# Optimization experiments

Measured on AMD Instinct MI355X. Metric: run time of the kernel, lower is better.

The kernel has to match this reference:

```python
import jax, jax.numpy as jnp
import numpy as np

B, S, D = 4, 4096, 1024
DFF = 4 * D
ACTIVE = 1024  # ceil(S * 0.25)


def setup_inputs() -> dict:
    key = jax.random.key(0)
    ks = jax.random.split(key, 4)
    x = jax.random.normal(ks[0], (B, S, D), dtype=jnp.float32)
    rw = jax.random.normal(ks[1], (D,), dtype=jnp.float32) * 0.02
    rb = jnp.zeros((1,), dtype=jnp.float32)
    w1 = jax.random.normal(ks[2], (D, DFF), dtype=jnp.float32) * 0.02
    b1 = jnp.zeros((DFF,), dtype=jnp.float32)
    w2 = jax.random.normal(ks[3], (DFF, D), dtype=jnp.float32) * 0.02
    b2 = jnp.zeros((D,), dtype=jnp.float32)
    return {"x": x, "rw": rw, "rb": rb, "w1": w1, "b1": b1,
            "w2": w2, "b2": b2, "active_tokens": ACTIVE}


def reference(x, rw, rb, w1, b1, w2, b2, active_tokens):
    b, s, d = x.shape
    # router: Linear(n_embd, 1) -> [B, S] scores
    scores = jnp.einsum('bsd,d->bs', x, rw) + rb[0]
    # top-k tokens per batch row
    _, idx = jax.lax.top_k(scores, active_tokens)          # [B, K] int32
    sel = jnp.take_along_axis(x, idx[..., None], axis=1)   # [B, K, D]
    # dense MLP on selected tokens (exact GELU as in torch nn.GELU)
    h = jax.nn.gelu(jnp.einsum('bkd,df->bkf', sel, w1) + b1, approximate=False)
    out = jnp.einsum('bkf,fd->bkd', h, w2) + b2            # [B, K, D]
    # sigmoid gate from router scores of selected tokens
    gates = jax.nn.sigmoid(jnp.take_along_axis(scores, idx, axis=1))  # [B, K]
    out = out * gates[..., None]
    # scatter back into zeros at selected positions
    flat_idx = (idx + jnp.arange(b, dtype=idx.dtype)[:, None] * s).reshape(-1)
    flat_out = jnp.zeros((b * s, d), dtype=out.dtype)
    flat_out = flat_out.at[flat_idx].set(out.reshape(-1, d))
    return flat_out.reshape(b, s, d)
```

## Files before the change

kernel.cpp:

```cpp
#include <hip/hip_runtime.h>
#include <hip/hip_bf16.h>
#include <cstdint>
#include <cstddef>

#define Bz 4
#define Sz 4096
#define Dz 1024
#define DFFz 4096
#define KACT 1024

typedef __bf16 bf16;
typedef __attribute__((ext_vector_type(8))) __bf16 bf16x8;
typedef __attribute__((ext_vector_type(4))) float f32x4;

__device__ __forceinline__ void async16(const void* g, void* l) {
  __builtin_amdgcn_global_load_lds(
      (const __attribute__((address_space(1))) void*)g,
      (__attribute__((address_space(3))) void*)l, 16, 0, 0);
}

__global__ void zero_out_k(float4* __restrict__ out, int n4) {
  int i = blockIdx.x * blockDim.x + threadIdx.x;
  int stride = gridDim.x * blockDim.x;
  for (; i < n4; i += stride) out[i] = make_float4(0.f, 0.f, 0.f, 0.f);
}

__global__ void router_k(const float* __restrict__ x, const float* __restrict__ rw,
                         const float* __restrict__ rb, float* __restrict__ scores) {
  int row = blockIdx.x * 4 + (threadIdx.x >> 6);
  int lane = threadIdx.x & 63;
  const float4* xr = (const float4*)(x + (size_t)row * Dz);
  const float4* wr = (const float4*)rw;
  float acc = 0.f;
#pragma unroll
  for (int i = 0; i < 4; ++i) {
    float4 a = xr[lane + i * 64];
    float4 w = wr[lane + i * 64];
    acc += a.x * w.x + a.y * w.y + a.z * w.z + a.w * w.w;
  }
#pragma unroll
  for (int d = 32; d; d >>= 1) acc += __shfl_down(acc, d, 64);
  if (lane == 0) scores[row] = acc + rb[0];
}

__global__ void transpose_cvt(const float* __restrict__ in, bf16* __restrict__ out,
                              int R, int C) {
  __shared__ float t[32][33];
  int c0 = blockIdx.x * 32, r0 = blockIdx.y * 32;
  int tx = threadIdx.x, ty = threadIdx.y;
#pragma unroll
  for (int i = 0; i < 32; i += 8) t[ty + i][tx] = in[(size_t)(r0 + ty + i) * C + c0 + tx];
  __syncthreads();
#pragma unroll
  for (int i = 0; i < 32; i += 8)
    out[(size_t)(c0 + ty + i) * R + r0 + tx] = (bf16)t[tx][ty + i];
}

__global__ void select_gather_k(const float* __restrict__ x, const float* __restrict__ scores,
                                int* __restrict__ cnt, int* __restrict__ sel_idx,
                                float* __restrict__ gates, bf16* __restrict__ Xsel) {
  int b = blockIdx.x >> 12;
  int s = blockIdx.x & (Sz - 1);
  const float* sc = scores + (size_t)b * Sz;
  float mine = sc[s];
  int tid = threadIdx.x;
  int c = 0;
  for (int t = tid; t < Sz; t += 256) {
    float o = sc[t];
    c += (o > mine) || (o == mine && t < s);
  }
#pragma unroll
  for (int d = 32; d; d >>= 1) c += __shfl_down(c, d, 64);
  __shared__ int red[4];
  __shared__ int rowbase;
  if ((tid & 63) == 0) red[tid >> 6] = c;
  __syncthreads();
  if (tid == 0) {
    int tot = red[0] + red[1] + red[2] + red[3];
    if (tot < KACT) {
      int pos = atomicAdd(cnt + b, 1);
      int m = b * KACT + pos;
      sel_idx[m] = s;
      gates[m] = 1.f / (1.f + expf(-mine));
      rowbase = m;
    } else {
      rowbase = -1;
    }
  }
  __syncthreads();
  int m = rowbase;
  if (m >= 0) {
    const float* xr = x + ((size_t)b * Sz + s) * Dz;
    bf16* xd = Xsel + (size_t)m * Dz;
    for (int i = tid; i < Dz; i += 256) xd[i] = (bf16)xr[i];
  }
}

__global__ __launch_bounds__(256) void gemm1_k(const bf16* __restrict__ A,
                                               const bf16* __restrict__ Bt,
                                               const float* __restrict__ bias,
                                               bf16* __restrict__ H) {
  constexpr int K = Dz, N = DFFz;
  __shared__ __align__(16) bf16 As[128 * 32];
  __shared__ __align__(16) bf16 Bs[128 * 32];
  const int tid = threadIdx.x;
  const int wave = tid >> 6, lane = tid & 63;
  const int quad = lane >> 4, l16 = lane & 15;
  const int m0 = blockIdx.y * 128, n0 = blockIdx.x * 128;
  const int wm = (wave >> 1) * 64, wn = (wave & 1) * 64;
  const int r0 = tid >> 2;
  const int kk = (tid & 3) * 8;

  f32x4 acc[4][4] = {};

  const bf16* Ag = A + (size_t)(m0 + r0) * K + kk;
  const bf16* Bg = Bt + (size_t)(n0 + r0) * K + kk;
  bf16* lAs0 = &As[wave * 512];
  bf16* lAs1 = &As[2048 + wave * 512];
  bf16* lBs0 = &Bs[wave * 512];
  bf16* lBs1 = &Bs[2048 + wave * 512];

  for (int k0 = 0; k0 < K; k0 += 32) {
    async16(Ag + k0, lAs0);
    async16(Ag + (size_t)64 * K + k0, lAs1);
    async16(Bg + k0, lBs0);
    async16(Bg + (size_t)64 * K + k0, lBs1);
    __syncthreads();
    bf16x8 af[4], bfr[4];
#pragma unroll
    for (int i = 0; i < 4; ++i) {
      af[i] = *(const bf16x8*)&As[(wm + i * 16 + l16) * 32 + quad * 8];
      bfr[i] = *(const bf16x8*)&Bs[(wn + i * 16 + l16) * 32 + quad * 8];
    }
#pragma unroll
    for (int mi = 0; mi < 4; ++mi)
#pragma unroll
      for (int ni = 0; ni < 4; ++ni)
        acc[mi][ni] = __builtin_amdgcn_mfma_f32_16x16x32_bf16(af[mi], bfr[ni], acc[mi][ni], 0, 0, 0);
    __syncthreads();
  }

#pragma unroll
  for (int mi = 0; mi < 4; ++mi) {
    int mbase = m0 + wm + mi * 16 + quad * 4;
#pragma unroll
    for (int ni = 0; ni < 4; ++ni) {
      int n = n0 + wn + ni * 16 + l16;
      float bn = bias[n];
#pragma unroll
      for (int r = 0; r < 4; ++r) {
        float z = acc[mi][ni][r] + bn;
        float g = 0.5f * z * (1.f + erff(z * 0.70710678118654752f));
        H[(size_t)(mbase + r) * N + n] = (bf16)g;
      }
    }
  }
}

__global__ __launch_bounds__(256) void gemm2_k(const bf16* __restrict__ A,
                                               const bf16* __restrict__ Bt,
                                               const float* __restrict__ bias,
                                               const int* __restrict__ sel_idx,
                                               const float* __restrict__ gates,
                                               float* __restrict__ out) {
  constexpr int K = DFFz, N = Dz;
  __shared__ __align__(16) bf16 As[128 * 32];
  __shared__ __align__(16) bf16 Bs[128 * 32];
  const int tid = threadIdx.x;
  const int wave = tid >> 6, lane = tid & 63;
  const int quad = lane >> 4, l16 = lane & 15;
  const int m0 = blockIdx.y * 128, n0 = blockIdx.x * 128;
  const int wm = (wave >> 1) * 64, wn = (wave & 1) * 64;
  const int r0 = tid >> 2;
  const int kk = (tid & 3) * 8;

  f32x4 acc[4][4] = {};

  const bf16* Ag = A + (size_t)(m0 + r0) * K + kk;
  const bf16* Bg = Bt + (size_t)(n0 + r0) * K + kk;
  bf16* lAs0 = &As[wave * 512];
  bf16* lAs1 = &As[2048 + wave * 512];
  bf16* lBs0 = &Bs[wave * 512];
  bf16* lBs1 = &Bs[2048 + wave * 512];

  for (int k0 = 0; k0 < K; k0 += 32) {
    async16(Ag + k0, lAs0);
    async16(Ag + (size_t)64 * K + k0, lAs1);
    async16(Bg + k0, lBs0);
    async16(Bg + (size_t)64 * K + k0, lBs1);
    __syncthreads();
    bf16x8 af[4], bfr[4];
#pragma unroll
    for (int i = 0; i < 4; ++i) {
      af[i] = *(const bf16x8*)&As[(wm + i * 16 + l16) * 32 + quad * 8];
      bfr[i] = *(const bf16x8*)&Bs[(wn + i * 16 + l16) * 32 + quad * 8];
    }
#pragma unroll
    for (int mi = 0; mi < 4; ++mi)
#pragma unroll
      for (int ni = 0; ni < 4; ++ni)
        acc[mi][ni] = __builtin_amdgcn_mfma_f32_16x16x32_bf16(af[mi], bfr[ni], acc[mi][ni], 0, 0, 0);
    __syncthreads();
  }

#pragma unroll
  for (int mi = 0; mi < 4; ++mi) {
#pragma unroll
    for (int r = 0; r < 4; ++r) {
      int m = m0 + wm + mi * 16 + quad * 4 + r;
      int b = m >> 10;
      int s = sel_idx[m];
      float gt = gates[m];
      float* orow = out + ((size_t)b * Sz + s) * Dz;
#pragma unroll
      for (int ni = 0; ni < 4; ++ni) {
        int n = n0 + wn + ni * 16 + l16;
        orow[n] = (acc[mi][ni][r] + bias[n]) * gt;
      }
    }
  }
}

extern "C" void kernel_launch(void* const* d_in, const int* in_sizes, int n_in,
                              void* d_out, int out_size, void* d_ws, size_t ws_size,
                              hipStream_t stream) {
  (void)in_sizes; (void)n_in; (void)out_size; (void)ws_size;
  const float* x  = (const float*)d_in[0];
  const float* rw = (const float*)d_in[1];
  const float* rb = (const float*)d_in[2];
  const float* w1 = (const float*)d_in[3];
  const float* b1 = (const float*)d_in[4];
  const float* w2 = (const float*)d_in[5];
  const float* b2 = (const float*)d_in[6];
  float* out = (float*)d_out;

  char* ws = (char*)d_ws;
  float* scores = (float*)ws;  ws += (size_t)Bz * Sz * 4;
  int*   sel_idx = (int*)ws;   ws += (size_t)Bz * KACT * 4;
  float* gates = (float*)ws;   ws += (size_t)Bz * KACT * 4;
  int*   cnt = (int*)ws;       ws += 256;
  bf16*  w1T = (bf16*)ws;      ws += (size_t)DFFz * Dz * 2;
  bf16*  w2T = (bf16*)ws;      ws += (size_t)Dz * DFFz * 2;
  bf16*  Xsel = (bf16*)ws;     ws += (size_t)Bz * KACT * Dz * 2;
  bf16*  H = (bf16*)ws;        ws += (size_t)Bz * KACT * DFFz * 2;

  hipMemsetAsync(cnt, 0, 16, stream);
  zero_out_k<<<8192, 256, 0, stream>>>((float4*)out, (Bz * Sz * Dz) / 4);
  router_k<<<(Bz * Sz) / 4, 256, 0, stream>>>(x, rw, rb, scores);
  transpose_cvt<<<dim3(DFFz / 32, Dz / 32), dim3(32, 8), 0, stream>>>(w1, w1T, Dz, DFFz);
  transpose_cvt<<<dim3(Dz / 32, DFFz / 32), dim3(32, 8), 0, stream>>>(w2, w2T, DFFz, Dz);
  select_gather_k<<<Bz * Sz, 256, 0, stream>>>(x, scores, cnt, sel_idx, gates, Xsel);
  gemm1_k<<<dim3(DFFz / 128, (Bz * KACT) / 128), 256, 0, stream>>>(Xsel, w1T, b1, H);
  gemm2_k<<<dim3(Dz / 128, (Bz * KACT) / 128), 256, 0, stream>>>(H, w2T, b2, sel_idx, gates, out);
}
```

Before: 358.6 us.

## Double-buffer GEMM LDS tiles and use rank-based slots in select_gather

The two GEMM kernels now use double-buffered LDS tiles. The next k-tile's async global-to-LDS loads are issued before computing on the current tile, with explicit vmcnt waits and barriers, so load latency overlaps the MFMA work. select_gather_k drops the atomic counter and its memset: each selected token writes to slot b*K + rank, and the row copy is vectorised to float4 loads and bf16x4 stores. LDS use per GEMM block doubles, and the hand-written waitcnt/barrier sequence depends on the compiler emitting the loads in the expected order.

New measurement: 352.4 us. Within noise of the previous version (-1.7%).

```diff
diff --git a/kernel.cpp b/kernel.cpp
--- a/kernel.cpp
+++ b/kernel.cpp
@@ -11,6 +11,7 @@
 
 typedef __bf16 bf16;
 typedef __attribute__((ext_vector_type(8))) __bf16 bf16x8;
+typedef __attribute__((ext_vector_type(4))) __bf16 bf16x4;
 typedef __attribute__((ext_vector_type(4))) float f32x4;
 
 __device__ __forceinline__ void async16(const void* g, void* l) {
@@ -57,8 +58,8 @@
 }
 
 __global__ void select_gather_k(const float* __restrict__ x, const float* __restrict__ scores,
-                                int* __restrict__ cnt, int* __restrict__ sel_idx,
-                                float* __restrict__ gates, bf16* __restrict__ Xsel) {
+                                int* __restrict__ sel_idx, float* __restrict__ gates,
+                                bf16* __restrict__ Xsel) {
   int b = blockIdx.x >> 12;
   int s = blockIdx.x & (Sz - 1);
   const float* sc = scores + (size_t)b * Sz;
@@ -72,74 +73,75 @@
 #pragma unroll
   for (int d = 32; d; d >>= 1) c += __shfl_down(c, d, 64);
   __shared__ int red[4];
-  __shared__ int rowbase;
   if ((tid & 63) == 0) red[tid >> 6] = c;
   __syncthreads();
+  int tot = red[0] + red[1] + red[2] + red[3];
+  if (tot >= KACT) return;
+  int m = b * KACT + tot;
   if (tid == 0) {
-    int tot = red[0] + red[1] + red[2] + red[3];
-    if (tot < KACT) {
-      int pos = atomicAdd(cnt + b, 1);
-      int m = b * KACT + pos;
-      sel_idx[m] = s;
-      gates[m] = 1.f / (1.f + expf(-mine));
-      rowbase = m;
-    } else {
-      rowbase = -1;
-    }
-  }
-  __syncthreads();
-  int m = rowbase;
-  if (m >= 0) {
-    const float* xr = x + ((size_t)b * Sz + s) * Dz;
-    bf16* xd = Xsel + (size_t)m * Dz;
-    for (int i = tid; i < Dz; i += 256) xd[i] = (bf16)xr[i];
-  }
-}
+    sel_idx[m] = s;
+    gates[m] = 1.f / (1.f + expf(-mine));
+  }
+  const float4* xr = (const float4*)(x + ((size_t)b * Sz + s) * Dz);
+  bf16x4* xd = (bf16x4*)(Xsel + (size_t)m * Dz);
+  float4 v = xr[tid];
+  bf16x4 o = {(bf16)v.x, (bf16)v.y, (bf16)v.z, (bf16)v.w};
+  xd[tid] = o;
+}
+
+#define GEMM_PREAMBLE(KV)                                                  \
+  __shared__ __align__(16) bf16 As[2][128 * 32];                           \
+  __shared__ __align__(16) bf16 Bs[2][128 * 32];                           \
+  const int tid = threadIdx.x;                                             \
+  const int wave = tid >> 6, lane = tid & 63;                              \
+  const int quad = lane >> 4, l16 = lane & 15;                             \
+  const int m0 = blockIdx.y * 128, n0 = blockIdx.x * 128;                  \
+  const int wm = (wave >> 1) * 64, wn = (wave & 1) * 64;                   \
+  const int r0 = tid >> 2;                                                 \
+  const int kk = (tid & 3) * 8;                                            \
+  f32x4 acc[4][4] = {};                                                    \
+  const bf16* Ag = A + (size_t)(m0 + r0) * KV + kk;                        \
+  const bf16* Bg = Bt + (size_t)(n0 + r0) * KV + kk;                       \
+  const int ldsoff = wave * 512;
+
+#define GEMM_ISSUE(KV, p, k0)                                              \
+  async16(Ag + (k0), &As[p][ldsoff]);                                      \
+  async16(Ag + (size_t)64 * KV + (k0), &As[p][2048 + ldsoff]);             \
+  async16(Bg + (k0), &Bs[p][ldsoff]);                                      \
+  async16(Bg + (size_t)64 * KV + (k0), &Bs[p][2048 + ldsoff]);
+
+#define GEMM_MAINLOOP(KV)                                                  \
+  GEMM_ISSUE(KV, 0, 0)                                                     \
+  int cur = 0;                                                             \
+  for (int it = 0; it < (KV) / 32; ++it) {                                 \
+    if (it + 1 < (KV) / 32) {                                              \
+      GEMM_ISSUE(KV, cur ^ 1, (it + 1) * 32)                               \
+      asm volatile("s_waitcnt vmcnt(4)\ns_barrier" ::: "memory");          \
+    } else {                                                               \
+      asm volatile("s_waitcnt vmcnt(0)\ns_barrier" ::: "memory");          \
+    }                                                                      \
+    bf16x8 af[4], bfr[4];                                                  \
+    _Pragma("unroll")                                                      \
+    for (int i = 0; i < 4; ++i) {                                          \
+      af[i] = *(const bf16x8*)&As[cur][(wm + i * 16 + l16) * 32 + quad * 8]; \
+      bfr[i] = *(const bf16x8*)&Bs[cur][(wn + i * 16 + l16) * 32 + quad * 8]; \
+    }                                                                      \
+    _Pragma("unroll")                                                      \
+    for (int mi = 0; mi < 4; ++mi)                                         \
+      _Pragma("unroll")                                                    \
+      for (int ni = 0; ni < 4; ++ni)                                       \
+        acc[mi][ni] = __builtin_amdgcn_mfma_f32_16x16x32_bf16(af[mi], bfr[ni], acc[mi][ni], 0, 0, 0); \
+    asm volatile("s_waitcnt lgkmcnt(0)\ns_barrier" ::: "memory");          \
+    cur ^= 1;                                                              \
+  }
 
 __global__ __launch_bounds__(256) void gemm1_k(const bf16* __restrict__ A,
                                                const bf16* __restrict__ Bt,
                                                const float* __restrict__ bias,
                                                bf16* __restrict__ H) {
   constexpr int K = Dz, N = DFFz;
-  __shared__ __align__(16) bf16 As[128 * 32];
-  __shared__ __align__(16) bf16 Bs[128 * 32];
-  const int tid = threadIdx.x;
-  const int wave = tid >> 6, lane = tid & 63;
-  const int quad = lane >> 4, l16 = lane & 15;
-  const int m0 = blockIdx.y * 128, n0 = blockIdx.x * 128;
-  const int wm = (wave >> 1) * 64, wn = (wave & 1) * 64;
-  const int r0 = tid >> 2;
-  const int kk = (tid & 3) * 8;
-
-  f32x4 acc[4][4] = {};
-
-  const bf16* Ag = A + (size_t)(m0 + r0) * K + kk;
-  const bf16* Bg = Bt + (size_t)(n0 + r0) * K + kk;
-  bf16* lAs0 = &As[wave * 512];
-  bf16* lAs1 = &As[2048 + wave * 512];
-  bf16* lBs0 = &Bs[wave * 512];
-  bf16* lBs1 = &Bs[2048 + wave * 512];
-
-  for (int k0 = 0; k0 < K; k0 += 32) {
-    async16(Ag + k0, lAs0);
-    async16(Ag + (size_t)64 * K + k0, lAs1);
-    async16(Bg + k0, lBs0);
-    async16(Bg + (size_t)64 * K + k0, lBs1);
-    __syncthreads();
-    bf16x8 af[4], bfr[4];
-#pragma unroll
-    for (int i = 0; i < 4; ++i) {
-      af[i] = *(const bf16x8*)&As[(wm + i * 16 + l16) * 32 + quad * 8];
-      bfr[i] = *(const bf16x8*)&Bs[(wn + i * 16 + l16) * 32 + quad * 8];
-    }
-#pragma unroll
-    for (int mi = 0; mi < 4; ++mi)
-#pragma unroll
-      for (int ni = 0; ni < 4; ++ni)
-        acc[mi][ni] = __builtin_amdgcn_mfma_f32_16x16x32_bf16(af[mi], bfr[ni], acc[mi][ni], 0, 0, 0);
-    __syncthreads();
-  }
-
+  GEMM_PREAMBLE(K)
+  GEMM_MAINLOOP(K)
 #pragma unroll
   for (int mi = 0; mi < 4; ++mi) {
     int mbase = m0 + wm + mi * 16 + quad * 4;
@@ -163,46 +165,9 @@
                                                const int* __restrict__ sel_idx,
                                                const float* __restrict__ gates,
                                                float* __restrict__ out) {
-  constexpr int K = DFFz, N = Dz;
-  __shared__ __align__(16) bf16 As[128 * 32];
-  __shared__ __align__(16) bf16 Bs[128 * 32];
-  const int tid = threadIdx.x;
-  const int wave = tid >> 6, lane = tid & 63;
-  const int quad = lane >> 4, l16 = lane & 15;
-  const int m0 = blockIdx.y * 128, n0 = blockIdx.x * 128;
-  const int wm = (wave >> 1) * 64, wn = (wave & 1) * 64;
-  const int r0 = tid >> 2;
-  const int kk = (tid & 3) * 8;
-
-  f32x4 acc[4][4] = {};
-
-  const bf16* Ag = A + (size_t)(m0 + r0) * K + kk;
-  const bf16* Bg = Bt + (size_t)(n0 + r0) * K + kk;
-  bf16* lAs0 = &As[wave * 512];
-  bf16* lAs1 = &As[2048 + wave * 512];
-  bf16* lBs0 = &Bs[wave * 512];
-  bf16* lBs1 = &Bs[2048 + wave * 512];
-
-  for (int k0 = 0; k0 < K; k0 += 32) {
-    async16(Ag + k0, lAs0);
-    async16(Ag + (size_t)64 * K + k0, lAs1);
-    async16(Bg + k0, lBs0);
-    async16(Bg + (size_t)64 * K + k0, lBs1);
-    __syncthreads();
-    bf16x8 af[4], bfr[4];
-#pragma unroll
-    for (int i = 0; i < 4; ++i) {
-      af[i] = *(const bf16x8*)&As[(wm + i * 16 + l16) * 32 + quad * 8];
-      bfr[i] = *(const bf16x8*)&Bs[(wn + i * 16 + l16) * 32 + quad * 8];
-    }
-#pragma unroll
-    for (int mi = 0; mi < 4; ++mi)
-#pragma unroll
-      for (int ni = 0; ni < 4; ++ni)
-        acc[mi][ni] = __builtin_amdgcn_mfma_f32_16x16x32_bf16(af[mi], bfr[ni], acc[mi][ni], 0, 0, 0);
-    __syncthreads();
-  }
-
+  constexpr int K = DFFz;
+  GEMM_PREAMBLE(K)
+  GEMM_MAINLOOP(K)
 #pragma unroll
   for (int mi = 0; mi < 4; ++mi) {
 #pragma unroll
@@ -238,18 +203,16 @@
   float* scores = (float*)ws;  ws += (size_t)Bz * Sz * 4;
   int*   sel_idx = (int*)ws;   ws += (size_t)Bz * KACT * 4;
   float* gates = (float*)ws;   ws += (size_t)Bz * KACT * 4;
-  int*   cnt = (int*)ws;       ws += 256;
   bf16*  w1T = (bf16*)ws;      ws += (size_t)DFFz * Dz * 2;
   bf16*  w2T = (bf16*)ws;      ws += (size_t)Dz * DFFz * 2;
   bf16*  Xsel = (bf16*)ws;     ws += (size_t)Bz * KACT * Dz * 2;
   bf16*  H = (bf16*)ws;        ws += (size_t)Bz * KACT * DFFz * 2;
 
-  hipMemsetAsync(cnt, 0, 16, stream);
   zero_out_k<<<8192, 256, 0, stream>>>((float4*)out, (Bz * Sz * Dz) / 4);
   router_k<<<(Bz * Sz) / 4, 256, 0, stream>>>(x, rw, rb, scores);
   transpose_cvt<<<dim3(DFFz / 32, Dz / 32), dim3(32, 8), 0, stream>>>(w1, w1T, Dz, DFFz);
   transpose_cvt<<<dim3(Dz / 32, DFFz / 32), dim3(32, 8), 0, stream>>>(w2, w2T, DFFz, Dz);
-  select_gather_k<<<Bz * Sz, 256, 0, stream>>>(x, scores, cnt, sel_idx, gates, Xsel);
+  select_gather_k<<<Bz * Sz, 256, 0, stream>>>(x, scores, sel_idx, gates, Xsel);
   gemm1_k<<<dim3(DFFz / 128, (Bz * KACT) / 128), 256, 0, stream>>>(Xsel, w1T, b1, H);
   gemm2_k<<<dim3(Dz / 128, (Bz * KACT) / 128), 256, 0, stream>>>(H, w2T, b2, sel_idx, gates, out);
 }
```

## Split-K gemm2 with atomic accumulation and rank-based deterministic token selection

Applied to the files above, without the earlier changes.

Gemm2 now splits its K dimension into four chunks along a third grid axis, so 1024 blocks run instead of 256 (256 CUs). Each chunk adds its partial result into the zeroed output with atomicAdd, and only the first chunk adds the gated bias. The select/gather kernel uses each token's rank as its slot, which removes the atomic counter and its memset, and the row conversion is vectorized to float4 loads. The split raises GPU occupancy for gemm2 at the cost of four-way atomic traffic on the output and a summation order that is no longer fixed.

After: 344.3 us. 4.0% less time.

```diff
diff --git a/kernel.cpp b/kernel.cpp
--- a/kernel.cpp
+++ b/kernel.cpp
@@ -11,6 +11,7 @@
 
 typedef __bf16 bf16;
 typedef __attribute__((ext_vector_type(8))) __bf16 bf16x8;
+typedef __attribute__((ext_vector_type(4))) __bf16 bf16x4;
 typedef __attribute__((ext_vector_type(4))) float f32x4;
 
 __device__ __forceinline__ void async16(const void* g, void* l) {
@@ -57,8 +58,8 @@
 }
 
 __global__ void select_gather_k(const float* __restrict__ x, const float* __restrict__ scores,
-                                int* __restrict__ cnt, int* __restrict__ sel_idx,
-                                float* __restrict__ gates, bf16* __restrict__ Xsel) {
+                                int* __restrict__ sel_idx, float* __restrict__ gates,
+                                bf16* __restrict__ Xsel) {
   int b = blockIdx.x >> 12;
   int s = blockIdx.x & (Sz - 1);
   const float* sc = scores + (size_t)b * Sz;
@@ -72,28 +73,20 @@
 #pragma unroll
   for (int d = 32; d; d >>= 1) c += __shfl_down(c, d, 64);
   __shared__ int red[4];
-  __shared__ int rowbase;
   if ((tid & 63) == 0) red[tid >> 6] = c;
   __syncthreads();
+  int tot = red[0] + red[1] + red[2] + red[3];
+  if (tot >= KACT) return;
+  int m = b * KACT + tot;
   if (tid == 0) {
-    int tot = red[0] + red[1] + red[2] + red[3];
-    if (tot < KACT) {
-      int pos = atomicAdd(cnt + b, 1);
-      int m = b * KACT + pos;
-      sel_idx[m] = s;
-      gates[m] = 1.f / (1.f + expf(-mine));
-      rowbase = m;
-    } else {
-      rowbase = -1;
-    }
-  }
-  __syncthreads();
-  int m = rowbase;
-  if (m >= 0) {
-    const float* xr = x + ((size_t)b * Sz + s) * Dz;
-    bf16* xd = Xsel + (size_t)m * Dz;
-    for (int i = tid; i < Dz; i += 256) xd[i] = (bf16)xr[i];
-  }
+    sel_idx[m] = s;
+    gates[m] = 1.f / (1.f + expf(-mine));
+  }
+  const float4* xr = (const float4*)(x + ((size_t)b * Sz + s) * Dz);
+  bf16x4* xd = (bf16x4*)(Xsel + (size_t)m * Dz);
+  float4 v = xr[tid];
+  bf16x4 o = {(bf16)v.x, (bf16)v.y, (bf16)v.z, (bf16)v.w};
+  xd[tid] = o;
 }
 
 __global__ __launch_bounds__(256) void gemm1_k(const bf16* __restrict__ A,
@@ -163,27 +156,29 @@
                                                const int* __restrict__ sel_idx,
                                                const float* __restrict__ gates,
                                                float* __restrict__ out) {
-  constexpr int K = DFFz, N = Dz;
+  constexpr int K = DFFz;
+  constexpr int KCH = 1024;
   __shared__ __align__(16) bf16 As[128 * 32];
   __shared__ __align__(16) bf16 Bs[128 * 32];
   const int tid = threadIdx.x;
   const int wave = tid >> 6, lane = tid & 63;
   const int quad = lane >> 4, l16 = lane & 15;
   const int m0 = blockIdx.y * 128, n0 = blockIdx.x * 128;
+  const int kc0 = blockIdx.z * KCH;
   const int wm = (wave >> 1) * 64, wn = (wave & 1) * 64;
   const int r0 = tid >> 2;
   const int kk = (tid & 3) * 8;
 
   f32x4 acc[4][4] = {};
 
-  const bf16* Ag = A + (size_t)(m0 + r0) * K + kk;
-  const bf16* Bg = Bt + (size_t)(n0 + r0) * K + kk;
+  const bf16* Ag = A + (size_t)(m0 + r0) * K + kc0 + kk;
+  const bf16* Bg = Bt + (size_t)(n0 + r0) * K + kc0 + kk;
   bf16* lAs0 = &As[wave * 512];
   bf16* lAs1 = &As[2048 + wave * 512];
   bf16* lBs0 = &Bs[wave * 512];
   bf16* lBs1 = &Bs[2048 + wave * 512];
 
-  for (int k0 = 0; k0 < K; k0 += 32) {
+  for (int k0 = 0; k0 < KCH; k0 += 32) {
     async16(Ag + k0, lAs0);
     async16(Ag + (size_t)64 * K + k0, lAs1);
     async16(Bg + k0, lBs0);
@@ -203,6 +198,7 @@
     __syncthreads();
   }
 
+  const bool addbias = (blockIdx.z == 0);
 #pragma unroll
   for (int mi = 0; mi < 4; ++mi) {
 #pragma unroll
@@ -215,7 +211,9 @@
 #pragma unroll
       for (int ni = 0; ni < 4; ++ni) {
         int n = n0 + wn + ni * 16 + l16;
-        orow[n] = (acc[mi][ni][r] + bias[n]) * gt;
+        float v = acc[mi][ni][r] * gt;
+        if (addbias) v += bias[n] * gt;
+        atomicAdd(&orow[n], v);
       }
     }
   }
@@ -238,18 +236,16 @@
   float* scores = (float*)ws;  ws += (size_t)Bz * Sz * 4;
   int*   sel_idx = (int*)ws;   ws += (size_t)Bz * KACT * 4;
   float* gates = (float*)ws;   ws += (size_t)Bz * KACT * 4;
-  int*   cnt = (int*)ws;       ws += 256;
   bf16*  w1T = (bf16*)ws;      ws += (size_t)DFFz * Dz * 2;
   bf16*  w2T = (bf16*)ws;      ws += (size_t)Dz * DFFz * 2;
   bf16*  Xsel = (bf16*)ws;     ws += (size_t)Bz * KACT * Dz * 2;
   bf16*  H = (bf16*)ws;        ws += (size_t)Bz * KACT * DFFz * 2;
 
-  hipMemsetAsync(cnt, 0, 16, stream);
   zero_out_k<<<8192, 256, 0, stream>>>((float4*)out, (Bz * Sz * Dz) / 4);
   router_k<<<(Bz * Sz) / 4, 256, 0, stream>>>(x, rw, rb, scores);
   transpose_cvt<<<dim3(DFFz / 32, Dz / 32), dim3(32, 8), 0, stream>>>(w1, w1T, Dz, DFFz);
   transpose_cvt<<<dim3(Dz / 32, DFFz / 32), dim3(32, 8), 0, stream>>>(w2, w2T, DFFz, Dz);
-  select_gather_k<<<Bz * Sz, 256, 0, stream>>>(x, scores, cnt, sel_idx, gates, Xsel);
+  select_gather_k<<<Bz * Sz, 256, 0, stream>>>(x, scores, sel_idx, gates, Xsel);
   gemm1_k<<<dim3(DFFz / 128, (Bz * KACT) / 128), 256, 0, stream>>>(Xsel, w1T, b1, H);
-  gemm2_k<<<dim3(Dz / 128, (Bz * KACT) / 128), 256, 0, stream>>>(H, w2T, b2, sel_idx, gates, out);
-}
+  gemm2_k<<<dim3(Dz / 128, (Bz * KACT) / 128, 4), 256, 0, stream>>>(H, w2T, b2, sel_idx, gates, out);
+}
```
